# Kernel optimization log

Hardware: AMD Instinct MI355X
Metric: run time of the kernel (lower is better)

The kernel has to match this reference:

```python
import jax, jax.numpy as jnp
import numpy as np

N_WORDS, MAX_CHARS = 32768, 16
WORD_DIM, CHAR_DIM, HIDDEN = 256, 64, 256
VOCAB = 256


def setup_inputs() -> dict:
    key = jax.random.key(0)
    ks = jax.random.split(key, 10)
    char_indices = jax.random.randint(ks[0], (N_WORDS, MAX_CHARS), 0, VOCAB)
    char_lengths = jax.random.randint(ks[1], (N_WORDS,), 1, MAX_CHARS + 1)
    word_emb = jax.random.normal(ks[2], (N_WORDS, WORD_DIM), dtype=jnp.float32)
    s = 0.05
    E_char = jax.random.normal(ks[3], (VOCAB, CHAR_DIM), dtype=jnp.float32) * s
    W_ih = jax.random.normal(ks[4], (4 * HIDDEN, CHAR_DIM), dtype=jnp.float32) * s
    W_hh = jax.random.normal(ks[5], (4 * HIDDEN, HIDDEN), dtype=jnp.float32) * s
    b_ih = jax.random.normal(ks[6], (4 * HIDDEN,), dtype=jnp.float32) * s
    b_hh = jax.random.normal(ks[7], (4 * HIDDEN,), dtype=jnp.float32) * s
    W_lin = jax.random.normal(ks[8], (WORD_DIM, WORD_DIM + HIDDEN), dtype=jnp.float32) * s
    b_lin = jax.random.normal(ks[9], (WORD_DIM,), dtype=jnp.float32) * s
    return dict(char_indices=char_indices, char_lengths=char_lengths,
                word_emb=word_emb, E_char=E_char, W_ih=W_ih, W_hh=W_hh,
                b_ih=b_ih, b_hh=b_hh, W_lin=W_lin, b_lin=b_lin)


def _lstm_last_hidden(x, lengths, W_ih, W_hh, b_ih, b_hh):
    # x: [N, T, E]; returns final hidden h at position length-1 per row.
    N, T, _ = x.shape
    H = W_hh.shape[1]
    x_proj = jnp.einsum('nte,ge->ntg', x, W_ih) + (b_ih + b_hh)  # [N, T, 4H]
    x_proj = jnp.transpose(x_proj, (1, 0, 2))                    # time-major [T, N, 4H]

    def step(carry, inp):
        h, c = carry
        xg, t = inp
        gates = xg + h @ W_hh.T
        i, f, g, o = jnp.split(gates, 4, axis=-1)
        i, f, o = jax.nn.sigmoid(i), jax.nn.sigmoid(f), jax.nn.sigmoid(o)
        g = jnp.tanh(g)
        c_new = f * c + i * g
        h_new = o * jnp.tanh(c_new)
        mask = (t < lengths)[:, None]  # freeze state past each word's length
        h = jnp.where(mask, h_new, h)
        c = jnp.where(mask, c_new, c)
        return (h, c), None

    h0 = jnp.zeros((N, H), dtype=x.dtype)
    c0 = jnp.zeros((N, H), dtype=x.dtype)
    (h, _), _ = jax.lax.scan(step, (h0, c0), (x_proj, jnp.arange(T)))
    return h


def reference(char_indices, char_lengths, word_emb, E_char, W_ih, W_hh,
              b_ih, b_hh, W_lin, b_lin):
    char_embedded = E_char[char_indices]                        # [N, T, E]
    h = _lstm_last_hidden(char_embedded, char_lengths, W_ih, W_hh, b_ih, b_hh)
    combined = jnp.concatenate([word_emb, h], axis=-1)          # [N, WORD+H]
    return jax.nn.relu(combined @ W_lin.T + b_lin)              # [N, WORD]
```

## Files before the change

### kernel.cpp

```cpp
#include <hip/hip_runtime.h>


#define NW 32768

typedef __attribute__((ext_vector_type(8))) short short8;
typedef __attribute__((ext_vector_type(4))) float f32x4;
typedef __attribute__((ext_vector_type(4))) int i32x4;
typedef __attribute__((ext_vector_type(8))) unsigned short u16x8;

#define MFMA16(a,b,c) __builtin_amdgcn_mfma_f32_16x16x32_bf16(a,b,c,0,0,0)
#define MFMAI8(a,b,c) __builtin_amdgcn_mfma_i32_16x16x64_i8(a,b,c,0,0,0)

#define O_ORDER 0
#define O_SLEN  131072
#define O_WPK   262144
#define O_USTP  524288
#define O_WLIN  528384
#define O_PX    790528
#define O_BH    1314816
#define O_BASE  1323008

__device__ inline unsigned short f2b(float f) {
  unsigned u = __builtin_bit_cast(unsigned, f);
  u = u + 0x7fffu + ((u >> 16) & 1u);
  return (unsigned short)(u >> 16);
}
__device__ inline float b2f(unsigned short u) {
  return __builtin_bit_cast(float, ((unsigned)u) << 16);
}
__device__ inline float fsigm(float x) {
  float e = __builtin_amdgcn_exp2f(-1.44269504f * x);
  return __builtin_amdgcn_rcpf(1.0f + e);
}
__device__ inline float ftanh(float x) {
  float e = __builtin_amdgcn_exp2f(2.88539008f * x);
  return 1.0f - 2.0f * __builtin_amdgcn_rcpf(e + 1.0f);
}

__global__ void k_prepA(const float* __restrict__ whh, const int* __restrict__ lens,
                        const float* __restrict__ wih, const float* __restrict__ ech,
                        const float* __restrict__ bih, const float* __restrict__ bhh,
                        unsigned char* __restrict__ ws) {
  int bid = blockIdx.x, tid = threadIdx.x;
  if (bid < 4) {
    int i = bid * 256 + tid;
    const f32x4* r4 = (const f32x4*)(whh + i * 256);
    float mx = 0.f;
    #pragma unroll 8
    for (int k4 = 0; k4 < 64; ++k4) {
      f32x4 v = r4[k4];
      mx = fmaxf(mx, fmaxf(fmaxf(fabsf(v[0]), fabsf(v[1])),
                           fmaxf(fabsf(v[2]), fabsf(v[3]))));
    }
    ((float*)(ws + O_USTP))[i] = mx / (127.f * 127.f);
    return;
  }
  if (bid < 132) {
    __shared__ int h[16];
    int b2 = bid - 4;
    if (tid < 16) h[tid] = 0;
    __syncthreads();
    int wid = b2 * 256 + tid;
    int l = lens[wid]; l = l < 1 ? 1 : (l > 16 ? 16 : l);
    atomicAdd(&h[l - 1], 1);
    __syncthreads();
    if (tid < 16) ((int*)(ws + O_BH))[b2 * 16 + tid] = h[tid];
    return;
  }
  int id = (bid - 132) * 256 + tid;
  int c = id >> 10, n = id & 1023;
  const f32x4* w4 = (const f32x4*)(wih + n * 64);
  const f32x4* e4 = (const f32x4*)(ech + c * 64);
  float acc = bih[n] + bhh[n];
  #pragma unroll
  for (int k4 = 0; k4 < 16; ++k4) {
    f32x4 a = w4[k4], e = e4[k4];
    acc += a[0] * e[0] + a[1] * e[1] + a[2] * e[2] + a[3] * e[3];
  }
  int g = n >> 8, hd = n & 255;
  int p = ((hd >> 5) << 4) | (hd & 15);
  int hs = (hd >> 4) & 1;
  ((unsigned short*)(ws + O_PX))[(((c << 7) + p) << 3) + (g << 1) + hs] = f2b(acc);
}

__global__ void k_prepB(const float* __restrict__ whh, const float* __restrict__ wlin,
                        unsigned char* __restrict__ ws) {
  int bid = blockIdx.x, tid = threadIdx.x;
  if (bid == 0) {
    __shared__ int tot[16], g[16];
    const int* bh = (const int*)(ws + O_BH);
    int* base = (int*)(ws + O_BASE);
    if (tid < 16) {
      int s = 0;
      for (int b = 0; b < 128; ++b) s += bh[b * 16 + tid];
      tot[tid] = s;
    }
    __syncthreads();
    if (tid == 0) { int a = 0; for (int i = 0; i < 16; ++i) { g[i] = a; a += tot[i]; } }
    __syncthreads();
    if (tid < 16) {
      int run = g[tid];
      for (int b = 0; b < 128; ++b) { base[b * 16 + tid] = run; run += bh[b * 16 + tid]; }
    }
    return;
  }
  int i = (bid - 1) * 256 + tid;
  if (i < 262144) {
    int j = i & 15, lane = (i >> 4) & 63, t2 = i >> 10;
    int nt = t2 & 7, u2 = t2 >> 3;
    int kb2 = u2 & 3, w = u2 >> 2;
    int n = (nt >> 1) * 256 + w * 32 + (nt & 1) * 16 + (lane & 15);
    int k = kb2 * 64 + (lane >> 4) * 16 + j;
    float v = whh[n * 256 + k];
    float ustep = ((const float*)(ws + O_USTP))[n] * 127.f;
    float qf = (ustep > 0.f) ? v / ustep : 0.f;
    int q = (int)__builtin_rintf(qf);
    q = q < -127 ? -127 : (q > 127 ? 127 : q);
    ((signed char*)(ws + O_WPK))[i] = (signed char)q;
    return;
  }
  int i2 = i - 262144;
  {
    int j = i2 & 7, lane = (i2 >> 3) & 63, t3 = i2 >> 9;
    int kf = t3 & 15, nn = t3 >> 4;
    int n = (nn >> 2) * 64 + (nn & 3) * 16 + (lane & 15);
    int k = kf * 32 + (lane >> 4) * 8 + j;
    ((unsigned short*)(ws + O_WLIN))[i2] = f2b(wlin[n * 512 + k]);
  }
}

__global__ void k_scatter(const int* __restrict__ lens, unsigned char* __restrict__ ws) {
  __shared__ int cnt[16];
  int t = threadIdx.x, b = blockIdx.x;
  if (t < 16) cnt[t] = 0;
  __syncthreads();
  int wid = b * 256 + t;
  int l = lens[wid]; l = l < 1 ? 1 : (l > 16 ? 16 : l);
  int rank = atomicAdd(&cnt[l - 1], 1);
  int p = ((const int*)(ws + O_BASE))[b * 16 + (l - 1)] + rank;
  ((int*)(ws + O_ORDER))[p] = wid;
  ((int*)(ws + O_SLEN))[p] = l;
}

__global__ __launch_bounds__(512)
__attribute__((amdgpu_waves_per_eu(2, 2)))
void k_main(
    const int* __restrict__ cidx, const float* __restrict__ wemb,
    const float* __restrict__ blin, float* __restrict__ outp,
    const unsigned char* __restrict__ ws) {
  __shared__ signed char Xb[2][4][4][64][16];
  __shared__ int CW[64][16];

  const int tid = threadIdx.x, b = blockIdx.x;
  const int w = tid >> 6, lane = tid & 63;
  const int q = lane >> 4, l15 = lane & 15;
  const int w16l = w * 16 + l15;
  const int kb2w = w >> 1;

  const int* order = (const int*)(ws + O_ORDER);
  const int* slen  = (const int*)(ws + O_SLEN);
  const signed char* wpk = (const signed char*)(ws + O_WPK);
  const float* upt = (const float*)(ws + O_USTP);
  const unsigned short* wlin = (const unsigned short*)(ws + O_WLIN);
  const unsigned short* pxt = (const unsigned short*)(ws + O_PX);

  i32x4 wreg[4][8];
  #pragma unroll
  for (int kb2 = 0; kb2 < 4; ++kb2)
    #pragma unroll
    for (int nt = 0; nt < 8; ++nt)
      wreg[kb2][nt] = *(const i32x4*)(wpk + (((w * 4 + kb2) * 8 + nt) * 64 + lane) * 16);

  float uq[8];
  #pragma unroll
  for (int nt = 0; nt < 8; ++nt) {
    int n = (nt >> 1) * 256 + w * 32 + (nt & 1) * 16 + l15;
    uq[nt] = upt[n];
  }
  const int mh = w >> 2, nw = w & 3;
  float blv[4];
  #pragma unroll
  for (int nt = 0; nt < 4; ++nt) blv[nt] = blin[nw * 64 + nt * 16 + l15];

  for (int sl = 0; sl < 2; ++sl) {
    const int s = sl ? (511 - b) : b;
    const int base = 64 * s;
    __syncthreads();
    {
      long* pz = (long*)&Xb[0][0][0][0][0];
      #pragma unroll
      for (int ii = 0; ii < 4; ++ii) pz[tid + 512 * ii] = 0L;
    }
    if (tid < 256) {
      int m = tid >> 2, part = tid & 3;
      int wid = order[base + m];
      *(i32x4*)&CW[m][part * 4] =
          __builtin_nontemporal_load((const i32x4*)(cidx + wid * 16 + part * 4));
    }
    int tmax[4]; unsigned lenpk[4];
    #pragma unroll
    for (int mt = 0; mt < 4; ++mt) {
      int pbm = base + 16 * mt;
      tmax[mt] = slen[pbm + 15];
      unsigned l0 = (unsigned)slen[pbm + q * 4 + 0];
      unsigned l1 = (unsigned)slen[pbm + q * 4 + 1];
      unsigned l2 = (unsigned)slen[pbm + q * 4 + 2];
      unsigned l3 = (unsigned)slen[pbm + q * 4 + 3];
      lenpk[mt] = l0 | (l1 << 8) | (l2 << 16) | (l3 << 24);
    }
    const int Tm = tmax[3];
    __syncthreads();

    float creg[4][2][4];
    unsigned hreg[4][2];
    #pragma unroll
    for (int mt = 0; mt < 4; ++mt)
      #pragma unroll
      for (int hs = 0; hs < 2; ++hs) {
        hreg[mt][hs] = 0u;
        #pragma unroll
        for (int r = 0; r < 4; ++r) creg[mt][hs][r] = 0.f;
      }

    for (int t = 0; t < Tm; ++t) {
      const int rd = t & 1, wb = rd ^ 1;
      #pragma unroll
      for (int mt = 0; mt < 4; ++mt) {
        if (mt != 3 && t >= tmax[mt]) continue;
        u16x8 pb8[4];
        #pragma unroll
        for (int r = 0; r < 4; ++r) {
          int cc = CW[mt * 16 + q * 4 + r][t] & 255;
          pb8[r] = *(const u16x8*)&pxt[(((cc << 7) + w16l)) << 3];
        }
        bool lv[4];
        #pragma unroll
        for (int r = 0; r < 4; ++r)
          lv[r] = t < (int)((lenpk[mt] >> (8 * r)) & 255u);
        #pragma unroll
        for (int hs = 0; hs < 2; ++hs) {
          i32x4 a0 = (i32x4)0, a1 = (i32x4)0, a2 = (i32x4)0, a3 = (i32x4)0;
          #pragma unroll
          for (int kb2 = 0; kb2 < 4; ++kb2) {
            i32x4 A = *(const i32x4*)&Xb[rd][mt][kb2][lane][0];
            a0 = MFMAI8(A, wreg[kb2][0 + hs], a0);
            a1 = MFMAI8(A, wreg[kb2][2 + hs], a1);
            a2 = MFMAI8(A, wreg[kb2][4 + hs], a2);
            a3 = MFMAI8(A, wreg[kb2][6 + hs], a3);
          }
          unsigned hp = 0;
          #pragma unroll
          for (int r = 0; r < 4; ++r) {
            float gi = (float)a0[r] * uq[0 + hs] + b2f(pb8[r][0 + hs]);
            float gf = (float)a1[r] * uq[2 + hs] + b2f(pb8[r][2 + hs]);
            float gg = (float)a2[r] * uq[4 + hs] + b2f(pb8[r][4 + hs]);
            float go = (float)a3[r] * uq[6 + hs] + b2f(pb8[r][6 + hs]);
            float si = fsigm(gi), sf = fsigm(gf);
            float sg = ftanh(gg), so = fsigm(go);
            float cold = creg[mt][hs][r];
            float cn = sf * cold + si * sg;
            float hn = so * ftanh(cn);
            creg[mt][hs][r] = lv[r] ? cn : cold;
            int hq = (int)__builtin_rintf(127.f * hn);
            unsigned ob = (hreg[mt][hs] >> (8 * r)) & 255u;
            unsigned nb = lv[r] ? ((unsigned)hq & 255u) : ob;
            hp |= nb << (8 * r);
          }
          hreg[mt][hs] = hp;
        }
      }

      #pragma unroll
      for (int mt = 0; mt < 4; ++mt) {
        if (mt != 3 && t >= tmax[mt]) continue;
        #pragma unroll
        for (int hs = 0; hs < 2; ++hs) {
          int row16 = 16 * ((w & 1) * 2 + hs);
          #pragma unroll
          for (int r = 0; r < 4; ++r)
            Xb[wb][mt][kb2w][(q * 4 + r) + row16][l15] =
                (signed char)((hreg[mt][hs] >> (8 * r)) & 255u);
        }
      }
      __syncthreads();
    }

    int widA[2];
    #pragma unroll
    for (int mi = 0; mi < 2; ++mi) widA[mi] = order[base + (2 * mh + mi) * 16 + l15];
    const int tb0 = (mh ? tmax[2] : tmax[0]) & 1;
    const int tb1 = (mh ? tmax[3] : tmax[1]) & 1;
    f32x4 fac[2][4];
    #pragma unroll
    for (int mi = 0; mi < 2; ++mi)
      #pragma unroll
      for (int nt = 0; nt < 4; ++nt) fac[mi][nt] = 0.0f;

    #pragma unroll
    for (int kf = 0; kf < 16; ++kf) {
      short8 Bn[4];
      #pragma unroll
      for (int nt = 0; nt < 4; ++nt)
        Bn[nt] = ((const short8*)wlin)[((nw * 4 + nt) * 16 + kf) * 64 + lane];
      short8 Am[2];
      #pragma unroll
      for (int mi = 0; mi < 2; ++mi) {
        if (kf < 8) {
          const f32x4* pa = (const f32x4*)(wemb + widA[mi] * 256 + kf * 32 + q * 8);
          f32x4 f0 = pa[0];
          f32x4 f1 = pa[1];
          short8 A;
          A[0] = (short)f2b(f0[0]); A[1] = (short)f2b(f0[1]);
          A[2] = (short)f2b(f0[2]); A[3] = (short)f2b(f0[3]);
          A[4] = (short)f2b(f1[0]); A[5] = (short)f2b(f1[1]);
          A[6] = (short)f2b(f1[2]); A[7] = (short)f2b(f1[3]);
          Am[mi] = A;
        } else {
          int mtv = 2 * mh + mi;
          int tb = mi ? tb1 : tb0;
          int hkb = (kf - 8) * 32 + q * 8;
          int kb2 = hkb >> 6, off = hkb & 63;
          long ch = *(const long*)&Xb[tb][mtv][kb2][l15 + 16 * (off >> 4)][off & 8];
          short8 A;
          #pragma unroll
          for (int j = 0; j < 8; ++j) {
            int v = (int)(signed char)((ch >> (8 * j)) & 255);
            A[j] = (short)f2b((float)v * (1.f / 127.f));
          }
          Am[mi] = A;
        }
      }
      #pragma unroll
      for (int mi = 0; mi < 2; ++mi)
        #pragma unroll
        for (int nt = 0; nt < 4; ++nt)
          fac[mi][nt] = MFMA16(Am[mi], Bn[nt], fac[mi][nt]);
    }
    #pragma unroll
    for (int mi = 0; mi < 2; ++mi) {
      #pragma unroll
      for (int r = 0; r < 4; ++r) {
        int wid = order[base + (2 * mh + mi) * 16 + q * 4 + r];
        float* po = outp + wid * 256 + nw * 64 + l15;
        #pragma unroll
        for (int nt = 0; nt < 4; ++nt) {
          float v = fac[mi][nt][r] + blv[nt];
          __builtin_nontemporal_store(v > 0.f ? v : 0.f, po + nt * 16);
        }
      }
    }
  }
}

extern "C" void kernel_launch(void* const* d_in, const int* in_sizes, int n_in,
                              void* d_out, int out_size, void* d_ws, size_t ws_size,
                              hipStream_t stream) {
  const int*   cidx = (const int*)d_in[0];
  const int*   clen = (const int*)d_in[1];
  const float* wemb = (const float*)d_in[2];
  const float* ech  = (const float*)d_in[3];
  const float* wih  = (const float*)d_in[4];
  const float* whh  = (const float*)d_in[5];
  const float* bih  = (const float*)d_in[6];
  const float* bhh  = (const float*)d_in[7];
  const float* wlin = (const float*)d_in[8];
  const float* blin = (const float*)d_in[9];
  float* outp = (float*)d_out;
  unsigned char* ws = (unsigned char*)d_ws;

  k_prepA<<<1156, 256, 0, stream>>>(whh, clen, wih, ech, bih, bhh, ws);
  k_prepB<<<1537, 256, 0, stream>>>(whh, wlin, ws);
  k_scatter<<<128, 256, 0, stream>>>(clen, ws);
  k_main<<<256, 512, 0, stream>>>(cidx, wemb, blin, outp, ws);
}
```

Measured before the change: 371.6 us.

## Interleave both LSTM slices in one time loop to overlap independent recurrences

Each block now runs its two 64-word slices (short and long length buckets) together in a single time loop, with separate double-buffered hidden-state tiles in dynamic shared memory. Interleaving the two independent recurrences is meant to hide MFMA and latency dependencies, and it halves the number of per-step barriers compared with running the slices one after the other. The short slice keeps its cell state packed as bf16 to save registers. The precomputed input projection layout changes to gate-interleaved u16x4, and the output GEMM moves after both recurrences. The trade-offs are higher register pressure, 72KB of shared memory, and reduced precision in the bf16 cell state.

```diff
diff --git a/kernel.cpp b/kernel.cpp
--- a/kernel.cpp
+++ b/kernel.cpp
@@ -6,7 +6,7 @@
 typedef __attribute__((ext_vector_type(8))) short short8;
 typedef __attribute__((ext_vector_type(4))) float f32x4;
 typedef __attribute__((ext_vector_type(4))) int i32x4;
-typedef __attribute__((ext_vector_type(8))) unsigned short u16x8;
+typedef __attribute__((ext_vector_type(4))) unsigned short u16x4;
 
 #define MFMA16(a,b,c) __builtin_amdgcn_mfma_f32_16x16x32_bf16(a,b,c,0,0,0)
 #define MFMAI8(a,b,c) __builtin_amdgcn_mfma_i32_16x16x64_i8(a,b,c,0,0,0)
@@ -77,10 +77,7 @@
     f32x4 a = w4[k4], e = e4[k4];
     acc += a[0] * e[0] + a[1] * e[1] + a[2] * e[2] + a[3] * e[3];
   }
-  int g = n >> 8, hd = n & 255;
-  int p = ((hd >> 5) << 4) | (hd & 15);
-  int hs = (hd >> 4) & 1;
-  ((unsigned short*)(ws + O_PX))[(((c << 7) + p) << 3) + (g << 1) + hs] = f2b(acc);
+  ((unsigned short*)(ws + O_PX))[((c << 8) + (n & 255)) * 4 + (n >> 8)] = f2b(acc);
 }
 
 __global__ void k_prepB(const float* __restrict__ whh, const float* __restrict__ wlin,
@@ -148,13 +145,14 @@
     const int* __restrict__ cidx, const float* __restrict__ wemb,
     const float* __restrict__ blin, float* __restrict__ outp,
     const unsigned char* __restrict__ ws) {
-  __shared__ signed char Xb[2][4][4][64][16];
-  __shared__ int CW[64][16];
+  extern __shared__ signed char smem[];
+  signed char (*Xb)[2][4][4][64][16] = (signed char (*)[2][4][4][64][16])smem;
+  int (*CW)[64][16] = (int (*)[64][16])(smem + 65536);
 
   const int tid = threadIdx.x, b = blockIdx.x;
   const int w = tid >> 6, lane = tid & 63;
   const int q = lane >> 4, l15 = lane & 15;
-  const int w16l = w * 16 + l15;
+  const int hd0 = w * 32 + l15;
   const int kb2w = w >> 1;
 
   const int* order = (const int*)(ws + O_ORDER);
@@ -178,118 +176,195 @@
     uq[nt] = upt[n];
   }
   const int mh = w >> 2, nw = w & 3;
+
+  const int baseA = 64 * b;
+  const int baseB = 64 * (511 - b);
+
+  {
+    long* pz = (long*)smem;
+    #pragma unroll
+    for (int ii = 0; ii < 4; ++ii) pz[tid + 512 * ii] = 0L;
+    #pragma unroll
+    for (int ii = 0; ii < 4; ++ii) pz[4096 + tid + 512 * ii] = 0L;
+  }
+  {
+    int sl = tid >> 8, r = tid & 255;
+    int m = r >> 2, part = r & 3;
+    int wid = order[(sl ? baseB : baseA) + m];
+    *(i32x4*)&CW[sl][m][part * 4] =
+        __builtin_nontemporal_load((const i32x4*)(cidx + wid * 16 + part * 4));
+  }
+  int tmA[4], tmB[4]; unsigned lpA[4], lpB[4];
+  #pragma unroll
+  for (int mt = 0; mt < 4; ++mt) {
+    int pa = baseA + 16 * mt, pb = baseB + 16 * mt;
+    tmA[mt] = __builtin_amdgcn_readfirstlane(slen[pa + 15]);
+    tmB[mt] = __builtin_amdgcn_readfirstlane(slen[pb + 15]);
+    unsigned a0 = (unsigned)slen[pa + q * 4 + 0], a1 = (unsigned)slen[pa + q * 4 + 1];
+    unsigned a2 = (unsigned)slen[pa + q * 4 + 2], a3 = (unsigned)slen[pa + q * 4 + 3];
+    lpA[mt] = a0 | (a1 << 8) | (a2 << 16) | (a3 << 24);
+    unsigned b0 = (unsigned)slen[pb + q * 4 + 0], b1 = (unsigned)slen[pb + q * 4 + 1];
+    unsigned b2 = (unsigned)slen[pb + q * 4 + 2], b3 = (unsigned)slen[pb + q * 4 + 3];
+    lpB[mt] = b0 | (b1 << 8) | (b2 << 16) | (b3 << 24);
+  }
+  const int TmB = tmB[3];
+  __syncthreads();
+
+  float    cregL[4][2][4];
+  unsigned hregL[4][2];
+  unsigned cregS[4][2][2];
+  unsigned hregS[4][2];
+  #pragma unroll
+  for (int mt = 0; mt < 4; ++mt)
+    #pragma unroll
+    for (int hs = 0; hs < 2; ++hs) {
+      hregL[mt][hs] = 0u; hregS[mt][hs] = 0u;
+      cregS[mt][hs][0] = 0u; cregS[mt][hs][1] = 0u;
+      #pragma unroll
+      for (int r = 0; r < 4; ++r) cregL[mt][hs][r] = 0.f;
+    }
+
+  for (int t = 0; t < TmB; ++t) {
+    const int rd = t & 1, wb = rd ^ 1;
+
+    #pragma unroll
+    for (int mt = 0; mt < 4; ++mt) {
+      if (mt != 3 && t >= tmB[mt]) continue;
+      int cc[4];
+      #pragma unroll
+      for (int r = 0; r < 4; ++r) cc[r] = CW[1][mt * 16 + q * 4 + r][t] & 255;
+      bool lv[4];
+      #pragma unroll
+      for (int r = 0; r < 4; ++r)
+        lv[r] = t < (int)((lpB[mt] >> (8 * r)) & 255u);
+      #pragma unroll
+      for (int hs = 0; hs < 2; ++hs) {
+        u16x4 pbv[4];
+        #pragma unroll
+        for (int r = 0; r < 4; ++r)
+          pbv[r] = *(const u16x4*)&pxt[((cc[r] << 8) + hd0 + hs * 16) * 4];
+        i32x4 a0 = (i32x4)0, a1 = (i32x4)0, a2 = (i32x4)0, a3 = (i32x4)0;
+        #pragma unroll
+        for (int kb2 = 0; kb2 < 4; ++kb2) {
+          i32x4 A = *(const i32x4*)&Xb[1][rd][mt][kb2][lane][0];
+          a0 = MFMAI8(A, wreg[kb2][0 + hs], a0);
+          a1 = MFMAI8(A, wreg[kb2][2 + hs], a1);
+          a2 = MFMAI8(A, wreg[kb2][4 + hs], a2);
+          a3 = MFMAI8(A, wreg[kb2][6 + hs], a3);
+        }
+        unsigned hp = 0;
+        #pragma unroll
+        for (int r = 0; r < 4; ++r) {
+          float gi = (float)a0[r] * uq[0 + hs] + b2f(pbv[r][0]);
+          float gf = (float)a1[r] * uq[2 + hs] + b2f(pbv[r][1]);
+          float gg = (float)a2[r] * uq[4 + hs] + b2f(pbv[r][2]);
+          float go = (float)a3[r] * uq[6 + hs] + b2f(pbv[r][3]);
+          float si = fsigm(gi), sf = fsigm(gf);
+          float sg = ftanh(gg), so = fsigm(go);
+          float cold = cregL[mt][hs][r];
+          float cn = sf * cold + si * sg;
+          float hn = so * ftanh(cn);
+          cregL[mt][hs][r] = lv[r] ? cn : cold;
+          int hq = (int)__builtin_rintf(127.f * hn);
+          unsigned ob = (hregL[mt][hs] >> (8 * r)) & 255u;
+          unsigned nb = lv[r] ? ((unsigned)hq & 255u) : ob;
+          hp |= nb << (8 * r);
+        }
+        hregL[mt][hs] = hp;
+      }
+    }
+
+    #pragma unroll
+    for (int mt = 0; mt < 4; ++mt) {
+      if (t >= tmA[mt]) continue;
+      int cc[4];
+      #pragma unroll
+      for (int r = 0; r < 4; ++r) cc[r] = CW[0][mt * 16 + q * 4 + r][t] & 255;
+      bool lv[4];
+      #pragma unroll
+      for (int r = 0; r < 4; ++r)
+        lv[r] = t < (int)((lpA[mt] >> (8 * r)) & 255u);
+      #pragma unroll
+      for (int hs = 0; hs < 2; ++hs) {
+        u16x4 pbv[4];
+        #pragma unroll
+        for (int r = 0; r < 4; ++r)
+          pbv[r] = *(const u16x4*)&pxt[((cc[r] << 8) + hd0 + hs * 16) * 4];
+        i32x4 a0 = (i32x4)0, a1 = (i32x4)0, a2 = (i32x4)0, a3 = (i32x4)0;
+        #pragma unroll
+        for (int kb2 = 0; kb2 < 4; ++kb2) {
+          i32x4 A = *(const i32x4*)&Xb[0][rd][mt][kb2][lane][0];
+          a0 = MFMAI8(A, wreg[kb2][0 + hs], a0);
+          a1 = MFMAI8(A, wreg[kb2][2 + hs], a1);
+          a2 = MFMAI8(A, wreg[kb2][4 + hs], a2);
+          a3 = MFMAI8(A, wreg[kb2][6 + hs], a3);
+        }
+        unsigned hp = 0;
+        float kept[4];
+        #pragma unroll
+        for (int r = 0; r < 4; ++r) {
+          unsigned cu = cregS[mt][hs][r >> 1];
+          float cold = b2f((unsigned short)((r & 1) ? (cu >> 16) : (cu & 0xffffu)));
+          float gi = (float)a0[r] * uq[0 + hs] + b2f(pbv[r][0]);
+          float gf = (float)a1[r] * uq[2 + hs] + b2f(pbv[r][1]);
+          float gg = (float)a2[r] * uq[4 + hs] + b2f(pbv[r][2]);
+          float go = (float)a3[r] * uq[6 + hs] + b2f(pbv[r][3]);
+          float si = fsigm(gi), sf = fsigm(gf);
+          float sg = ftanh(gg), so = fsigm(go);
+          float cn = sf * cold + si * sg;
+          float hn = so * ftanh(cn);
+          kept[r] = lv[r] ? cn : cold;
+          int hq = (int)__builtin_rintf(127.f * hn);
+          unsigned ob = (hregS[mt][hs] >> (8 * r)) & 255u;
+          unsigned nb = lv[r] ? ((unsigned)hq & 255u) : ob;
+          hp |= nb << (8 * r);
+        }
+        cregS[mt][hs][0] = (unsigned)f2b(kept[0]) | ((unsigned)f2b(kept[1]) << 16);
+        cregS[mt][hs][1] = (unsigned)f2b(kept[2]) | ((unsigned)f2b(kept[3]) << 16);
+        hregS[mt][hs] = hp;
+      }
+    }
+
+    #pragma unroll
+    for (int mt = 0; mt < 4; ++mt) {
+      if (mt != 3 && t >= tmB[mt]) continue;
+      #pragma unroll
+      for (int hs = 0; hs < 2; ++hs) {
+        int row16 = 16 * ((w & 1) * 2 + hs);
+        #pragma unroll
+        for (int r = 0; r < 4; ++r)
+          Xb[1][wb][mt][kb2w][(q * 4 + r) + row16][l15] =
+              (signed char)((hregL[mt][hs] >> (8 * r)) & 255u);
+      }
+    }
+    #pragma unroll
+    for (int mt = 0; mt < 4; ++mt) {
+      if (t >= tmA[mt]) continue;
+      #pragma unroll
+      for (int hs = 0; hs < 2; ++hs) {
+        int row16 = 16 * ((w & 1) * 2 + hs);
+        #pragma unroll
+        for (int r = 0; r < 4; ++r)
+          Xb[0][wb][mt][kb2w][(q * 4 + r) + row16][l15] =
+              (signed char)((hregS[mt][hs] >> (8 * r)) & 255u);
+      }
+    }
+    __syncthreads();
+  }
+
   float blv[4];
   #pragma unroll
   for (int nt = 0; nt < 4; ++nt) blv[nt] = blin[nw * 64 + nt * 16 + l15];
 
-  for (int sl = 0; sl < 2; ++sl) {
-    const int s = sl ? (511 - b) : b;
-    const int base = 64 * s;
-    __syncthreads();
-    {
-      long* pz = (long*)&Xb[0][0][0][0][0];
-      #pragma unroll
-      for (int ii = 0; ii < 4; ++ii) pz[tid + 512 * ii] = 0L;
-    }
-    if (tid < 256) {
-      int m = tid >> 2, part = tid & 3;
-      int wid = order[base + m];
-      *(i32x4*)&CW[m][part * 4] =
-          __builtin_nontemporal_load((const i32x4*)(cidx + wid * 16 + part * 4));
-    }
-    int tmax[4]; unsigned lenpk[4];
-    #pragma unroll
-    for (int mt = 0; mt < 4; ++mt) {
-      int pbm = base + 16 * mt;
-      tmax[mt] = slen[pbm + 15];
-      unsigned l0 = (unsigned)slen[pbm + q * 4 + 0];
-      unsigned l1 = (unsigned)slen[pbm + q * 4 + 1];
-      unsigned l2 = (unsigned)slen[pbm + q * 4 + 2];
-      unsigned l3 = (unsigned)slen[pbm + q * 4 + 3];
-      lenpk[mt] = l0 | (l1 << 8) | (l2 << 16) | (l3 << 24);
-    }
-    const int Tm = tmax[3];
-    __syncthreads();
-
-    float creg[4][2][4];
-    unsigned hreg[4][2];
-    #pragma unroll
-    for (int mt = 0; mt < 4; ++mt)
-      #pragma unroll
-      for (int hs = 0; hs < 2; ++hs) {
-        hreg[mt][hs] = 0u;
-        #pragma unroll
-        for (int r = 0; r < 4; ++r) creg[mt][hs][r] = 0.f;
-      }
-
-    for (int t = 0; t < Tm; ++t) {
-      const int rd = t & 1, wb = rd ^ 1;
-      #pragma unroll
-      for (int mt = 0; mt < 4; ++mt) {
-        if (mt != 3 && t >= tmax[mt]) continue;
-        u16x8 pb8[4];
-        #pragma unroll
-        for (int r = 0; r < 4; ++r) {
-          int cc = CW[mt * 16 + q * 4 + r][t] & 255;
-          pb8[r] = *(const u16x8*)&pxt[(((cc << 7) + w16l)) << 3];
-        }
-        bool lv[4];
-        #pragma unroll
-        for (int r = 0; r < 4; ++r)
-          lv[r] = t < (int)((lenpk[mt] >> (8 * r)) & 255u);
-        #pragma unroll
-        for (int hs = 0; hs < 2; ++hs) {
-          i32x4 a0 = (i32x4)0, a1 = (i32x4)0, a2 = (i32x4)0, a3 = (i32x4)0;
-          #pragma unroll
-          for (int kb2 = 0; kb2 < 4; ++kb2) {
-            i32x4 A = *(const i32x4*)&Xb[rd][mt][kb2][lane][0];
-            a0 = MFMAI8(A, wreg[kb2][0 + hs], a0);
-            a1 = MFMAI8(A, wreg[kb2][2 + hs], a1);
-            a2 = MFMAI8(A, wreg[kb2][4 + hs], a2);
-            a3 = MFMAI8(A, wreg[kb2][6 + hs], a3);
-          }
-          unsigned hp = 0;
-          #pragma unroll
-          for (int r = 0; r < 4; ++r) {
-            float gi = (float)a0[r] * uq[0 + hs] + b2f(pb8[r][0 + hs]);
-            float gf = (float)a1[r] * uq[2 + hs] + b2f(pb8[r][2 + hs]);
-            float gg = (float)a2[r] * uq[4 + hs] + b2f(pb8[r][4 + hs]);
-            float go = (float)a3[r] * uq[6 + hs] + b2f(pb8[r][6 + hs]);
-            float si = fsigm(gi), sf = fsigm(gf);
-            float sg = ftanh(gg), so = fsigm(go);
-            float cold = creg[mt][hs][r];
-            float cn = sf * cold + si * sg;
-            float hn = so * ftanh(cn);
-            creg[mt][hs][r] = lv[r] ? cn : cold;
-            int hq = (int)__builtin_rintf(127.f * hn);
-            unsigned ob = (hreg[mt][hs] >> (8 * r)) & 255u;
-            unsigned nb = lv[r] ? ((unsigned)hq & 255u) : ob;
-            hp |= nb << (8 * r);
-          }
-          hreg[mt][hs] = hp;
-        }
-      }
-
-      #pragma unroll
-      for (int mt = 0; mt < 4; ++mt) {
-        if (mt != 3 && t >= tmax[mt]) continue;
-        #pragma unroll
-        for (int hs = 0; hs < 2; ++hs) {
-          int row16 = 16 * ((w & 1) * 2 + hs);
-          #pragma unroll
-          for (int r = 0; r < 4; ++r)
-            Xb[wb][mt][kb2w][(q * 4 + r) + row16][l15] =
-                (signed char)((hreg[mt][hs] >> (8 * r)) & 255u);
-        }
-      }
-      __syncthreads();
-    }
-
+  #pragma unroll
+  for (int sl2 = 0; sl2 < 2; ++sl2) {
+    const int base = sl2 ? baseB : baseA;
+    const int t0 = sl2 ? tmB[mh ? 2 : 0] : tmA[mh ? 2 : 0];
+    const int t1 = sl2 ? tmB[mh ? 3 : 1] : tmA[mh ? 3 : 1];
+    const int tb0 = t0 & 1, tb1 = t1 & 1;
     int widA[2];
     #pragma unroll
     for (int mi = 0; mi < 2; ++mi) widA[mi] = order[base + (2 * mh + mi) * 16 + l15];
-    const int tb0 = (mh ? tmax[2] : tmax[0]) & 1;
-    const int tb1 = (mh ? tmax[3] : tmax[1]) & 1;
     f32x4 fac[2][4];
     #pragma unroll
     for (int mi = 0; mi < 2; ++mi)
@@ -320,7 +395,7 @@
           int tb = mi ? tb1 : tb0;
           int hkb = (kf - 8) * 32 + q * 8;
           int kb2 = hkb >> 6, off = hkb & 63;
-          long ch = *(const long*)&Xb[tb][mtv][kb2][l15 + 16 * (off >> 4)][off & 8];
+          long ch = *(const long*)&Xb[sl2][tb][mtv][kb2][l15 + 16 * (off >> 4)][off & 15];
           short8 A;
           #pragma unroll
           for (int j = 0; j < 8; ++j) {
@@ -371,5 +446,5 @@
   k_prepA<<<1156, 256, 0, stream>>>(whh, clen, wih, ech, bih, bhh, ws);
   k_prepB<<<1537, 256, 0, stream>>>(whh, wlin, ws);
   k_scatter<<<128, 256, 0, stream>>>(clen, ws);
-  k_main<<<256, 512, 0, stream>>>(cidx, wemb, blin, outp, ws);
-}
+  k_main<<<256, 512, 73728, stream>>>(cidx, wemb, blin, outp, ws);
+}
```

Measured after the change: 473.9 us. +27.5%, slower.
